# Kernel optimization log

Hardware: AMD Instinct MI355X
Metric: run time of the kernel (lower is better)

## Reference

```python
import jax, jax.numpy as jnp
import numpy as np

DEPTH = 10
LEAF = 2 ** DEPTH          # 1024 leaves
NODE_NUM = 2 * LEAF - 1    # 2047
N = NODE_NUM + 1           # 2048 nodes incl. global node 0
ATTN = 4
D = 128
B = 8
L = 2


def _trace_children(ni):
    terms = []
    s, e = ni << 1, (ni << 1) | 1
    while s <= NODE_NUM and e <= NODE_NUM:
        terms.extend(range(s, e + 1))
        s <<= 1
        e = (e << 1) | 1
    return terms


def _trace_left(si):
    ni, cd, terms, stop = si + LEAF, DEPTH, [], False
    while not stop:
        cs = ni - ATTN + 1 - ((ni - ATTN + 1) & 1)
        stop = cs < 2 ** cd
        cs = max(2 ** cd, cs)
        terms.extend(range(cs, ni + 1))
        ni = (cs - 1) >> 1
        cd -= 1
    return terms


def _trace_right(ei):
    ni, cd, terms, stop = ei + LEAF, DEPTH, [], False
    while not stop:
        ce = ni + ATTN - 1 + ((ni - ATTN) & 1)
        stop = ce >= 2 ** (cd + 1)
        ce = min(2 ** (cd + 1) - 1, ce)
        terms.extend(range(ni, ce + 1))
        ni = (ce + 1) >> 1
        cd -= 1
    return terms


def _build_edges():
    src, dst = [], []
    for ni in range(1, NODE_NUM + 1):
        if ni < LEAF:
            t = _trace_children(ni)
        else:
            t = _trace_left(ni - LEAF) + _trace_right(ni - LEAF)
        src.extend(t)
        dst.extend([ni] * len(t))
    e = np.stack([np.asarray(src, np.int64), np.asarray(dst, np.int64)])  # [2, E]
    off = np.arange(B, dtype=np.int64) * N
    eb = (e[:, None, :] + off[None, :, None]).reshape(2, -1)  # batch-offset like _fetch_edge_data
    return eb.astype(np.int32)


def setup_inputs() -> dict:
    key = jax.random.key(0)
    k0, k1, k2 = jax.random.split(key, 3)
    s = 1.0 / np.sqrt(D)
    return {
        "elements": jax.random.normal(k0, (B, LEAF, D), jnp.float32),
        "ln_gamma": jnp.ones((L, D), jnp.float32),
        "ln_beta": jnp.zeros((L, D), jnp.float32),
        "w_nei": (jax.random.normal(k1, (L, D, D), jnp.float32) * s),
        "b_nei": jnp.zeros((L, D), jnp.float32),
        "w_root": (jax.random.normal(k2, (L, D, D), jnp.float32) * s),
        "edge_index": jnp.asarray(_build_edges()),
    }


def _sinusoid(pos, d):
    # ArbitraryPositionEncoder: sinusoidal encoding over (possibly negative) positions
    half = d // 2
    inv = jnp.exp(-jnp.arange(half, dtype=jnp.float32) * (np.log(10000.0) / half))
    ang = pos[:, None] * inv[None, :]  # [n, half]
    return jnp.stack([jnp.sin(ang), jnp.cos(ang)], -1).reshape(pos.shape[0], d)


def reference(elements, ln_gamma, ln_beta, w_nei, b_nei, w_root, edge_index):
    Bx, leaf, d = elements.shape
    depth = int(np.log2(leaf))
    # bottom-up tree compression (mean of two children)
    cur = elements
    levels = [cur]
    for _ in range(depth):
        cur = 0.5 * (cur[:, 0::2] + cur[:, 1::2])
        levels.append(cur)
    # node ordering: [global node 0 (=-1), root (level 0), ..., leaves (level depth)]
    node_feat = jnp.concatenate(
        [jnp.full((Bx, 1, d), -1.0, elements.dtype)] + levels[::-1], axis=1)  # [B, N, D]
    n = node_feat.shape[1]
    # positional encoding: vertical = floor(log2(idx)), horizontal = idx - 2^vertical
    idx = jnp.arange(n, dtype=jnp.float32)
    vpos = jnp.floor(jnp.log2(jnp.where(idx == 0, 0.5, idx)))
    hpos = idx - jnp.exp2(vpos)
    enc = jnp.concatenate([_sinusoid(hpos, d // 2), _sinusoid(vpos, d // 2)], -1)  # [N, D]
    x = (node_feat + enc[None]).reshape(Bx * n, d)
    src, dst = edge_index[0], edge_index[1]
    nseg = Bx * n
    deg = jnp.maximum(
        jax.ops.segment_sum(jnp.ones(src.shape, jnp.float32), dst, num_segments=nseg), 1.0)
    # DeepGCNLayer res+ blocks with SAGEConv (mean aggr)
    for l in range(ln_gamma.shape[0]):
        mu = jnp.mean(x, -1, keepdims=True)
        var = jnp.mean((x - mu) ** 2, -1, keepdims=True)
        h = (x - mu) * jax.lax.rsqrt(var + 1e-5) * ln_gamma[l] + ln_beta[l]
        h = jax.nn.gelu(h, approximate=False)
        agg = jax.ops.segment_sum(h[src], dst, num_segments=nseg) / deg[:, None]
        h = agg @ w_nei[l] + b_nei[l] + h @ w_root[l]
        x = x + h
    return x.reshape(Bx, n, d)
```

## Files before the change

kernel.cpp:

```cpp
#include <hip/hip_runtime.h>
#include <hip/hip_bf16.h>

#define LEAFN 1024
#define NN    2048
#define BATCH 8
#define DD    128
#define ROWS  (BATCH*NN)
#define AHS   384
#define NB    256
#define NT    1024

#define LOG1E4_OVER_32 0.28782313662425575f

#define SLACK 9
#define CSTRIDE 136
#define AGGL_OFF 54672
#define RED_OFF  63376
#define RED2_OFF 64400

typedef __bf16 bf16x8 __attribute__((ext_vector_type(8)));
typedef float  floatx4 __attribute__((ext_vector_type(4)));
typedef float  floatx2 __attribute__((ext_vector_type(2)));

__device__ __forceinline__ float bf2f(unsigned short u) {
// ... 144 lines not shown
      float4 q0 = *(float4*)rowp;
      float4 q1 = *(float4*)(rowp + 4);
      float4 q2 = *(float4*)(rowp + 8);
      float4 q3 = *(float4*)(rowp + 12);
      float v[16] = {q0.x, q0.y, q0.z, q0.w, q1.x, q1.y, q1.z, q1.w,
                     q2.x, q2.y, q2.z, q2.w, q3.x, q3.y, q3.z, q3.w};
      float s1 = 0.f, s2 = 0.f;
#pragma unroll
      for (int j = 0; j < 16; ++j) { s1 += v[j]; s2 += v[j] * v[j]; }
      s1 += __shfl_xor(s1, 1); s2 += __shfl_xor(s2, 1);
      s1 += __shfl_xor(s1, 2); s2 += __shfl_xor(s2, 2);
      s1 += __shfl_xor(s1, 4); s2 += __shfl_xor(s2, 4);
      float mu = s1 * (1.0f / 128.0f);
      float var = s2 * (1.0f / 128.0f) - mu * mu;
      float rinv = rsqrtf(var + 1e-5f);
      int k = rr + 1, lv = 31 - __clz(k);
      int g = ((16 + s) << lv) | (k - (1 << lv));
      __attribute__((aligned(16))) unsigned short o[16];
      float hv[16];
#pragma unroll
      for (int j = 0; j < 16; ++j) {
        hv[j] = gelu((v[j] - mu) * rinv * gamma[dp + j] + beta[dp + j]);
        o[j] = f2bf(hv[j]);
      }
      *(float4*)rowp        = make_float4(hv[0], hv[1], hv[2], hv[3]);
      *(float4*)(rowp + 4)  = make_float4(hv[4], hv[5], hv[6], hv[7]);
      *(float4*)(rowp + 8)  = make_float4(hv[8], hv[9], hv[10], hv[11]);
      *(float4*)(rowp + 12) = make_float4(hv[12], hv[13], hv[14], hv[15]);
      unsigned short* dst = &ah[(size_t)(b * NN + g) * AHS + 128 + dp];
      *(uint4*)&dst[0] = *(uint4*)&o[0];
      *(uint4*)&dst[8] = *(uint4*)&o[8];
    }
  }
  __syncthreads();
  for (int lv = 5; lv >= 0; --lv) {
    int nk = 1 << lv;
    float inv = 1.0f / (float)((1 << (7 - lv)) - 2);
    for (int idx = tid; idx < nk * 32; idx += NT) {
      int k = nk + (idx >> 5);
      int j = idx & 31;
      floatx4 S = smv[(2 * k - 1) * 32 + j] + smv[(2 * k) * 32 + j];
      if (lv < 5) S = S + smv[(4 * k - 1) * 32 + j] + smv[(4 * k + 1) * 32 + j];
      smv[(2 * k - 1) * 32 + j] = S;
      int g = ((16 + s) << lv) | (k - nk);
      ushort4 o;
      o.x = f2bf(S[0] * inv); o.y = f2bf(S[1] * inv);
      o.z = f2bf(S[2] * inv); o.w = f2bf(S[3] * inv);
      *(ushort4*)&ah[(size_t)(b * NN + g) * AHS + j * 4] = o;
    }
    __syncthreads();
  }
  if (tid < 32)
    ((floatx4*)&sroot[(size_t)(b * 16 + s) * DD])[tid] = smv[32 + tid];
}

__device__ __forceinline__ void ph_top(char* smemc, int b,
                                       const float* __restrict__ lvl4,
                                       unsigned short* __restrict__ ah,
                                       const float* __restrict__ gamma,
                                       const float* __restrict__ beta) {
  float (*xs)[DD] = (float(*)[DD])smemc;
  int tid = threadIdx.x;
  if (tid < 128) {
    int d = tid;
    float v[16];
    for (int j = 0; j < 16; ++j) v[j] = lvl4[(b * 16 + j) * DD + d];
    for (int j = 0; j < 8; ++j) v[j] = 0.5f * (v[2 * j] + v[2 * j + 1]);
    for (int j = 0; j < 8; ++j) xs[8 + j][d] = v[j] + enc_val(8 + j, d);
    for (int j = 0; j < 4; ++j) v[j] = 0.5f * (v[2 * j] + v[2 * j + 1]);
    for (int j = 0; j < 4; ++j) xs[4 + j][d] = v[j] + enc_val(4 + j, d);
    for (int j = 0; j < 2; ++j) v[j] = 0.5f * (v[2 * j] + v[2 * j + 1]);
    for (int j = 0; j < 2; ++j) xs[2 + j][d] = v[j] + enc_val(2 + j, d);
    v[0] = 0.5f * (v[0] + v[1]);
    xs[1][d] = v[0] + enc_val(1, d);
    xs[0][d] = -1.0f + enc_val(0, d);
  }
  __syncthreads();
  if (tid < 128) {
    int rr = tid >> 3, sub = tid & 7, dp = sub * 16;
    float w[16], s1 = 0.f, s2 = 0.f;
#pragma unroll
    for (int j = 0; j < 16; ++j) { w[j] = xs[rr][dp + j]; s1 += w[j]; s2 += w[j] * w[j]; }
    s1 += __shfl_xor(s1, 1); s2 += __shfl_xor(s2, 1);
    s1 += __shfl_xor(s1, 2); s2 += __shfl_xor(s2, 2);
    s1 += __shfl_xor(s1, 4); s2 += __shfl_xor(s2, 4);
    float mu = s1 * (1.0f / 128.0f);
    float var = s2 * (1.0f / 128.0f) - mu * mu;
    float rinv = rsqrtf(var + 1e-5f);
    __attribute__((aligned(16))) unsigned short o[16];
#pragma unroll
    for (int j = 0; j < 16; ++j)
      o[j] = f2bf(gelu((w[j] - mu) * rinv * gamma[dp + j] + beta[dp + j]));
    unsigned short* dst = &ah[(size_t)(b * NN + rr) * AHS + 128 + dp];
    *(uint4*)&dst[0] = *(uint4*)&o[0];
    *(uint4*)&dst[8] = *(uint4*)&o[8];
  }
  __syncthreads();
}

__device__ __forceinline__ void ph_aggsub(char* smemc, int b, int s,
                                          unsigned short* ah,
                                          float* __restrict__ sroot) {
  floatx4 (*S)[32] = (floatx4(*)[32])smemc;
  int tid = threadIdx.x;
  for (int idx = tid; idx < 32 * 32; idx += NT) {
    int k = 32 + (idx >> 5), q = idx & 31;
    int c = (16 + s) * 64 + (2 * k - 64);
    size_t a0 = (size_t)(b * NN + c) * AHS + 256 + q * 4;
    ushort4 u0 = *(const ushort4*)&ah[a0];
    ushort4 u1 = *(const ushort4*)&ah[a0 + AHS];
    floatx4 v;
    v[0] = bf2f(u0.x) + bf2f(u1.x);
    v[1] = bf2f(u0.y) + bf2f(u1.y);
    v[2] = bf2f(u0.z) + bf2f(u1.z);
    v[3] = bf2f(u0.w) + bf2f(u1.w);
    S[k][q] = v;
    int g = (16 + s) * 32 + (k - 32);
    int r = b * NN + g;
    ushort4 o;
    o.x = f2bf(v[0] * 0.5f); o.y = f2bf(v[1] * 0.5f);
    o.z = f2bf(v[2] * 0.5f); o.w = f2bf(v[3] * 0.5f);
    *(ushort4*)&ah[(size_t)r * AHS + q * 4] = o;
  }
  __syncthreads();
  for (int lv = 4; lv >= 0; --lv) {
    int nk = 1 << lv;
    float inv = 1.0f / (float)((1 << (7 - lv)) - 2);
    for (int idx = tid; idx < nk * 32; idx += NT) {
      int k = nk + (idx >> 5), q = idx & 31;
      int c = ((16 + s) << (lv + 1)) | (2 * k - 2 * nk);
      size_t a0 = (size_t)(b * NN + c) * AHS + 256 + q * 4;
      ushort4 u0 = *(const ushort4*)&ah[a0];
      ushort4 u1 = *(const ushort4*)&ah[a0 + AHS];
      floatx4 sc0 = S[2 * k][q], sc1 = S[2 * k + 1][q];
      floatx4 v;
      v[0] = bf2f(u0.x) + bf2f(u1.x) + sc0[0] + sc1[0];
      v[1] = bf2f(u0.y) + bf2f(u1.y) + sc0[1] + sc1[1];
      v[2] = bf2f(u0.z) + bf2f(u1.z) + sc0[2] + sc1[2];
      v[3] = bf2f(u0.w) + bf2f(u1.w) + sc0[3] + sc1[3];
      S[k][q] = v;
      int g = ((16 + s) << lv) | (k - nk);
      int r = b * NN + g;
      ushort4 o;
      o.x = f2bf(v[0] * inv); o.y = f2bf(v[1] * inv);
      o.z = f2bf(v[2] * inv); o.w = f2bf(v[3] * inv);
      *(ushort4*)&ah[(size_t)r * AHS + q * 4] = o;
    }
    __syncthreads();
  }
  for (int q = tid; q < 32; q += NT)
    ((floatx4*)sroot)[(size_t)(b * 16 + s) * 32 + q] = S[1][q];
}

__device__ __forceinline__ void ph_leafagg(char* smemc, int b, int jb,
                                           const int* __restrict__ srcv,
                                           const int* __restrict__ s0a,
                                           const int* __restrict__ s1a,
                                           const unsigned short* __restrict__ eoff,
                                           unsigned short* ah, int hoff) {
  unsigned short* cache = (unsigned short*)smemc;
  int tid = threadIdx.x;
  int lo[11], wd[11], off[11];
  int acc_off = 0;
#pragma unroll
  for (int cd = 10; cd >= 1; --cd) {
    win_cd(jb, cd, lo[cd], wd[cd]);
    off[cd] = acc_off;
    acc_off += wd[cd];
  }
#pragma unroll
  for (int cd = 10; cd >= 1; --cd) {
    int w = wd[cd];
    for (int t = tid; t < w * 16; t += NT) {
      int row = t >> 4, seg = t & 15;
      *(uint4*)&cache[(off[cd] + row) * CSTRIDE + seg * 8] =
          *(const uint4*)&ah[(size_t)(b * NN + lo[cd] + row) * AHS + hoff + seg * 8];
    }
  }
  __syncthreads();

  int leaf = tid >> 5, half = (tid >> 4) & 1, c = tid & 15;
  int r = b * NN + 1024 + jb * 32 + leaf;
  int e0 = s0a[r], e1 = s1a[r];
  int n = e1 - e0;
  int mid = e0 + (n >> 1);
  int ebeg = half ? mid : e0;
  int eend = half ? e1 : mid;
  int cb = c * 16;
  floatx2 a0 = {0.f, 0.f}, a1 = {0.f, 0.f}, a2 = {0.f, 0.f}, a3 = {0.f, 0.f};
  auto one = [&](int ei) {
    unsigned o = eoff[ei];
    uint4 u;
    if (o != 0xFFFFu)
      u = *(const uint4*)(smemc + o + cb);
    else {
      int g = srcv[ei] - b * NN;
      u = *(const uint4*)&ah[(size_t)(b * NN + g) * AHS + hoff + c * 8];
    }
    a0 += bfpair(u.x); a1 += bfpair(u.y); a2 += bfpair(u.z); a3 += bfpair(u.w);
  };
  int e = ebeg;
  for (; e + 4 <= eend; e += 4) {
    unsigned o0 = eoff[e], o1 = eoff[e + 1], o2 = eoff[e + 2], o3 = eoff[e + 3];
    if (!((((o0 + 1) | (o1 + 1) | (o2 + 1) | (o3 + 1)) >> 16))) {
      uint4 u0 = *(const uint4*)(smemc + o0 + cb);
      uint4 u1 = *(const uint4*)(smemc + o1 + cb);
      uint4 u2 = *(const uint4*)(smemc + o2 + cb);
      uint4 u3 = *(const uint4*)(smemc + o3 + cb);
      a0 += bfpair(u0.x); a1 += bfpair(u0.y); a2 += bfpair(u0.z); a3 += bfpair(u0.w);
      a0 += bfpair(u1.x); a1 += bfpair(u1.y); a2 += bfpair(u1.z); a3 += bfpair(u1.w);
      a0 += bfpair(u2.x); a1 += bfpair(u2.y); a2 += bfpair(u2.z); a3 += bfpair(u2.w);
      a0 += bfpair(u3.x); a1 += bfpair(u3.y); a2 += bfpair(u3.z); a3 += bfpair(u3.w);
    } else {
      one(e); one(e + 1); one(e + 2); one(e + 3);
    }
  }
  for (; e < eend; ++e) one(e);
  a0[0] += __shfl_xor(a0[0], 16); a0[1] += __shfl_xor(a0[1], 16);
  a1[0] += __shfl_xor(a1[0], 16); a1[1] += __shfl_xor(a1[1], 16);
  a2[0] += __shfl_xor(a2[0], 16); a2[1] += __shfl_xor(a2[1], 16);
  a3[0] += __shfl_xor(a3[0], 16); a3[1] += __shfl_xor(a3[1], 16);
  if (!half) {
    float inv = 1.0f / (float)max(n, 1);
    unsigned short* aggl = (unsigned short*)(smemc + AGGL_OFF);
    __attribute__((aligned(16))) unsigned short o[8];
    o[0] = f2bf(a0[0] * inv); o[1] = f2bf(a0[1] * inv);
    o[2] = f2bf(a1[0] * inv); o[3] = f2bf(a1[1] * inv);
    o[4] = f2bf(a2[0] * inv); o[5] = f2bf(a2[1] * inv);
    o[6] = f2bf(a3[0] * inv); o[7] = f2bf(a3[1] * inv);
    *(uint4*)&aggl[leaf * CSTRIDE + c * 8] = *(uint4*)&o[0];
  }
}

__device__ __forceinline__ void ph_topfin(int b,
                                          const float* __restrict__ sroot,
                                          unsigned short* ah, int hoff) {
  int d = threadIdx.x;
  float S16[16], h16[16], Sv[16];
#pragma unroll
  for (int j = 0; j < 16; ++j) S16[j] = sroot[(size_t)(b * 16 + j) * DD + d];
#pragma unroll
  for (int j = 0; j < 16; ++j)
    h16[j] = bf2f(ah[(size_t)(b * NN + 16 + j) * AHS + hoff + d]);
#pragma unroll
  for (int k = 8; k < 16; ++k)
    Sv[k] = h16[2 * k - 16] + h16[2 * k - 15] + S16[2 * k - 16] + S16[2 * k - 15];
#pragma unroll
  for (int k = 7; k >= 1; --k)
    Sv[k] = bf2f(ah[(size_t)(b * NN + 2 * k) * AHS + hoff + d]) +
            bf2f(ah[(size_t)(b * NN + 2 * k + 1) * AHS + hoff + d]) +
            Sv[2 * k] + Sv[2 * k + 1];
#pragma unroll
  for (int k = 1; k < 16; ++k) {
    int dv = 31 - __clz(k);
    float inv = 1.0f / (float)((1 << (11 - dv)) - 2);
    ah[(size_t)(b * NN + k) * AHS + d] = f2bf(Sv[k] * inv);
  }
  ah[(size_t)(b * NN) * AHS + d] = f2bf(0.0f);
}

__device__ __forceinline__ void ph_gemm32(char* redc, const unsigned short* aggl,
                                          int rowbase, unsigned short* ah,
                                          const unsigned short* __restrict__ wfl,
                                          const float* __restrict__ bn,
                                          float* __restrict__ x, int hoff_in,
                                          const float* __restrict__ gamma,
                                          const float* __restrict__ beta,
                                          float* xc, int first_layer) {
  int wave = threadIdx.x >> 6, lane = threadIdx.x & 63;
  bool act = wave < 8;
  int wl = wave & 7;
  int mt = wl >> 2, nq = wl & 3;
  int r0 = rowbase + mt * 16;
  int m = lane & 15, q = lane >> 4;
  floatx4 acc[2];
  acc[0] = (floatx4){0.f, 0.f, 0.f, 0.f};
  acc[1] = (floatx4){0.f, 0.f, 0.f, 0.f};
  if (act) {
    const unsigned short* arow = ah + (size_t)(r0 + m) * AHS + q * 8;
    const bf16x8* B = (const bf16x8*)wfl + lane;
#pragma unroll
    for (int kc = 0; kc < 8; ++kc) {
      bf16x8 a0;
      if (kc < 4)
        a0 = *(const bf16x8*)&aggl[(mt * 16 + m) * CSTRIDE + kc * 32 + q * 8];
      else
        a0 = *(const bf16x8*)(arow + hoff_in + (kc - 4) * 32);
#pragma unroll
      for (int ci = 0; ci < 2; ++ci) {
        bf16x8 bb = B[(kc * 8 + nq * 2 + ci) * 64];
        acc[ci] = __builtin_amdgcn_mfma_f32_16x16x32_bf16(a0, bb, acc[ci], 0, 0, 0);
      }
    }
  }
  if (first_layer) {
    float s1[4] = {0.f, 0.f, 0.f, 0.f}, s2[4] = {0.f, 0.f, 0.f, 0.f};
    if (act) {
#pragma unroll
      for (int ci = 0; ci < 2; ++ci) {
        int col = (nq * 2 + ci) * 16 + m;
        float bias = bn[col];
#pragma unroll
        for (int r = 0; r < 4; ++r) {
          int row = r0 + q * 4 + r;
          float v = x[(size_t)row * DD + col] + acc[ci][r] + bias;
          xc[ci * 4 + r] = v;
          s1[r] += v; s2[r] += v * v;
        }
      }
#pragma unroll
      for (int r = 0; r < 4; ++r) {
        s1[r] += __shfl_xor(s1[r], 1); s2[r] += __shfl_xor(s2[r], 1);
        s1[r] += __shfl_xor(s1[r], 2); s2[r] += __shfl_xor(s2[r], 2);
        s1[r] += __shfl_xor(s1[r], 4); s2[r] += __shfl_xor(s2[r], 4);
        s1[r] += __shfl_xor(s1[r], 8); s2[r] += __shfl_xor(s2[r], 8);
      }
    }
    float* red = (float*)redc;
    int rl = mt * 16 + q * 4;
    __syncthreads();
    if (act && m == 0) {
#pragma unroll
      for (int r = 0; r < 4; ++r) {
        red[(rl + r) * 4 + nq] = s1[r];
        red[128 + (rl + r) * 4 + nq] = s2[r];
      }
    }
    __syncthreads();
    if (act) {
      float mu[4], rv[4];
#pragma unroll
      for (int r = 0; r < 4; ++r) {
        float t1 = red[(rl + r) * 4] + red[(rl + r) * 4 + 1] +
                   red[(rl + r) * 4 + 2] + red[(rl + r) * 4 + 3];
        float t2 = red[128 + (rl + r) * 4] + red[128 + (rl + r) * 4 + 1] +
                   red[128 + (rl + r) * 4 + 2] + red[128 + (rl + r) * 4 + 3];
        mu[r] = t1 * (1.0f / 128.0f);
        float var = t2 * (1.0f / 128.0f) - mu[r] * mu[r];
        rv[r] = rsqrtf(var + 1e-5f);
      }
#pragma unroll
      for (int ci = 0; ci < 2; ++ci) {
        int col = (nq * 2 + ci) * 16 + m;
        float gm = gamma[col], bt = beta[col];
#pragma unroll
        for (int r = 0; r < 4; ++r) {
          int row = r0 + q * 4 + r;
          float hh = gelu((xc[ci * 4 + r] - mu[r]) * rv[r] * gm + bt);
          ah[(size_t)row * AHS + 256 + col] = f2bf(hh);
        }
      }
    }
  } else {
    if (act) {
#pragma unroll
      for (int ci = 0; ci < 2; ++ci) {
        int col = (nq * 2 + ci) * 16 + m;
        float bias = bn[col];
#pragma unroll
        for (int r = 0; r < 4; ++r) {
          int row = r0 + q * 4 + r;
          x[(size_t)row * DD + col] = xc[ci * 4 + r] + acc[ci][r] + bias;
        }
      }
    }
  }
}

__device__ __forceinline__ void ph_gemm32s(char* redc, int b, int sb, int tbase,
                                           unsigned short* ah,
                                           const unsigned short* __restrict__ wfl,
                                           const float* __restrict__ bn,
                                           float* __restrict__ x, int hoff_in,
                                           const float* __restrict__ gamma,
                                           const float* __restrict__ beta,
                                           float* xc, int first_layer,
                                           const float* __restrict__ gx) {
  int wave = threadIdx.x >> 6, lane = threadIdx.x & 63;
  bool act = wave >= 8;
  int wl = wave & 7;
  int mt = wl >> 2, nq = wl & 3;
  int m = lane & 15, q = lane >> 4;
  int tA = tbase + mt * 16 + m;
  int kA = (tA == 63) ? 1 : tA + 1;
  int lvA = 31 - __clz(kA);
  int rowA = b * NN + (((16 + sb) << lvA) | (kA - (1 << lvA)));
  int rowO[4];
#pragma unroll
  for (int r = 0; r < 4; ++r) {
    int t = tbase + mt * 16 + q * 4 + r;
    int k = (t == 63) ? 1 : t + 1;
    int lv = 31 - __clz(k);
    rowO[r] = b * NN + (((16 + sb) << lv) | (k - (1 << lv)));
  }
  floatx4 acc[2];
  acc[0] = (floatx4){0.f, 0.f, 0.f, 0.f};
  acc[1] = (floatx4){0.f, 0.f, 0.f, 0.f};
  if (act) {
    const unsigned short* arow = ah + (size_t)rowA * AHS + q * 8;
    const bf16x8* B = (const bf16x8*)wfl + lane;
#pragma unroll
    for (int kc = 0; kc < 8; ++kc) {
      int koff = (kc < 4) ? kc * 32 : hoff_in + (kc - 4) * 32;
      bf16x8 a0 = *(const bf16x8*)(arow + koff);
#pragma unroll
      for (int ci = 0; ci < 2; ++ci) {
        bf16x8 bb = B[(kc * 8 + nq * 2 + ci) * 64];
        acc[ci] = __builtin_amdgcn_mfma_f32_16x16x32_bf16(a0, bb, acc[ci], 0, 0, 0);
      }
    }
  }
  if (first_layer) {
    float s1[4] = {0.f, 0.f, 0.f, 0.f}, s2[4] = {0.f, 0.f, 0.f, 0.f};
    if (act) {
#pragma unroll
      for (int ci = 0; ci < 2; ++ci) {
        int col = (nq * 2 + ci) * 16 + m;
        float bias = bn[col];
#pragma unroll
        for (int r = 0; r < 4; ++r) {
          float x0 = gx ? gx[(size_t)rowO[r] * DD + col] : xc[ci * 4 + r];
          float v = x0 + acc[ci][r] + bias;
          xc[ci * 4 + r] = v;
          s1[r] += v; s2[r] += v * v;
        }
      }
#pragma unroll
      for (int r = 0; r < 4; ++r) {
        s1[r] += __shfl_xor(s1[r], 1); s2[r] += __shfl_xor(s2[r], 1);
        s1[r] += __shfl_xor(s1[r], 2); s2[r] += __shfl_xor(s2[r], 2);
        s1[r] += __shfl_xor(s1[r], 4); s2[r] += __shfl_xor(s2[r], 4);
        s1[r] += __shfl_xor(s1[r], 8); s2[r] += __shfl_xor(s2[r], 8);
      }
    }
    float* red = (float*)redc;
    int rl = mt * 16 + q * 4;
    __syncthreads();
    if (act && m == 0) {
#pragma unroll
      for (int r = 0; r < 4; ++r) {
        red[(rl + r) * 4 + nq] = s1[r];
        red[128 + (rl + r) * 4 + nq] = s2[r];
      }
    }
    __syncthreads();
    if (act) {
      float mu[4], rv[4];
#pragma unroll
      for (int r = 0; r < 4; ++r) {
        float t1 = red[(rl + r) * 4] + red[(rl + r) * 4 + 1] +
                   red[(rl + r) * 4 + 2] + red[(rl + r) * 4 + 3];
        float t2 = red[128 + (rl + r) * 4] + red[128 + (rl + r) * 4 + 1] +
                   red[128 + (rl + r) * 4 + 2] + red[128 + (rl + r) * 4 + 3];
        mu[r] = t1 * (1.0f / 128.0f);
        float var = t2 * (1.0f / 128.0f) - mu[r] * mu[r];
        rv[r] = rsqrtf(var + 1e-5f);
      }
#pragma unroll
      for (int ci = 0; ci < 2; ++ci) {
        int col = (nq * 2 + ci) * 16 + m;
        float gm = gamma[col], bt = beta[col];
#pragma unroll
        for (int r = 0; r < 4; ++r) {
          float hh = gelu((xc[ci * 4 + r] - mu[r]) * rv[r] * gm + bt);
          ah[(size_t)rowO[r] * AHS + 256 + col] = f2bf(hh);
        }
      }
    }
  } else {
    if (act) {
#pragma unroll
      for (int ci = 0; ci < 2; ++ci) {
        int col = (nq * 2 + ci) * 16 + m;
        float bias = bn[col];
#pragma unroll
        for (int r = 0; r < 4; ++r)
          x[(size_t)rowO[r] * DD + col] = xc[ci * 4 + r] + acc[ci][r] + bias;
      }
    }
  }
}

__device__ __forceinline__ void ph_gemm16t(char* redc, int b,
                                           unsigned short* ah,
                                           const unsigned short* __restrict__ wfl,
                                           const float* __restrict__ bn,
                                           float* __restrict__ x, int hoff_in,
                                           const float* __restrict__ gamma,
                                           const float* __restrict__ beta,
                                           float* xc, int first_layer) {
  int ct = threadIdx.x >> 6, lane = threadIdx.x & 63;
  bool act = ct < 8;
  int m = lane & 15, q = lane >> 4;
  floatx4 acc = (floatx4){0.f, 0.f, 0.f, 0.f};
  int col = (ct & 7) * 16 + m;
  if (act) {
    const unsigned short* arow = ah + (size_t)(b * NN + m) * AHS + q * 8;
    const bf16x8* B = (const bf16x8*)wfl + lane;
#pragma unroll
    for (int kc = 0; kc < 8; ++kc) {
      int koff = (kc < 4) ? kc * 32 : hoff_in + (kc - 4) * 32;
      bf16x8 a0 = *(const bf16x8*)(arow + koff);
      bf16x8 bb = B[(kc * 8 + ct) * 64];
      acc = __builtin_amdgcn_mfma_f32_16x16x32_bf16(a0, bb, acc, 0, 0, 0);
    }
  }
  if (first_layer) {
    float s1[4] = {0.f, 0.f, 0.f, 0.f}, s2[4] = {0.f, 0.f, 0.f, 0.f};
    float bias = act ? bn[col] : 0.f;
    if (act) {
#pragma unroll
      for (int r = 0; r < 4; ++r) {
        float v = xc[r] + acc[r] + bias;
        xc[r] = v; s1[r] = v; s2[r] = v * v;
      }
#pragma unroll
      for (int r = 0; r < 4; ++r) {
        s1[r] += __shfl_xor(s1[r], 1); s2[r] += __shfl_xor(s2[r], 1);
        s1[r] += __shfl_xor(s1[r], 2); s2[r] += __shfl_xor(s2[r], 2);
        s1[r] += __shfl_xor(s1[r], 4); s2[r] += __shfl_xor(s2[r], 4);
        s1[r] += __shfl_xor(s1[r], 8); s2[r] += __shfl_xor(s2[r], 8);
      }
    }
    float* red = (float*)redc;
    __syncthreads();
    if (act && m == 0) {
#pragma unroll
      for (int r = 0; r < 4; ++r) {
        red[(q * 4 + r) * 8 + ct] = s1[r];
        red[128 + (q * 4 + r) * 8 + ct] = s2[r];
      }
    }
    __syncthreads();
    if (act) {
#pragma unroll
      for (int r = 0; r < 4; ++r) {
        float t1 = 0.f, t2 = 0.f;
#pragma unroll
        for (int j = 0; j < 8; ++j) {
          t1 += red[(q * 4 + r) * 8 + j];
          t2 += red[128 + (q * 4 + r) * 8 + j];
        }
        float mu = t1 * (1.0f / 128.0f);
        float var = t2 * (1.0f / 128.0f) - mu * mu;
        float rv = rsqrtf(var + 1e-5f);
        float hh = gelu((xc[r] - mu) * rv * gamma[col] + beta[col]);
        ah[(size_t)(b * NN + q * 4 + r) * AHS + 256 + col] = f2bf(hh);
      }
    }
  } else {
    if (act) {
      float bias = bn[col];
#pragma unroll
      for (int r = 0; r < 4; ++r)
        x[(size_t)(b * NN + q * 4 + r) * DD + col] = xc[r] + acc[r] + bias;
    }
  }
}

__global__ __launch_bounds__(NT, 1) void k_mega(
    const float* __restrict__ elements, const float* __restrict__ ln_gamma,
    const float* __restrict__ ln_beta, const float* __restrict__ w_nei,
    const float* __restrict__ b_nei, const float* __restrict__ w_root,
    const int* __restrict__ srcv, const int* __restrict__ dstv, int E,
    float* __restrict__ x, int* s0a, int* s1a, float* lvl4, float* sroot,
    unsigned short* wf, unsigned short* ah, unsigned short* eoff, int* bar) {
  __shared__ __align__(16) char smem[65536];
  int bid = blockIdx.x, tid = threadIdx.x;
  int b = bid & 7, gb = bid >> 3;
  int Eb = E >> 3;
  unsigned short* wfg = wf + (size_t)b * 65536;
  float xcl[8], xci[8], xct[4];
  int wv = tid >> 6;

  if (gb < 16) {
    ph_tree(smem, b, gb, elements, x, lvl4, ah, ln_gamma, ln_beta, sroot, xci, bar);
  } else if (gb < 24) {
    int base = b * Eb;
    for (int i = base + (gb - 16) * NT + tid; i < base + Eb; i += 8 * NT) {
      int dv = dstv[i];
      if (i == 0 || dstv[i - 1] != dv) s0a[dv] = i;
      if (i == base + Eb - 1 || dstv[i + 1] != dv) s1a[dv] = i + 1;
    }
    for (int i = base + (gb - 16) * NT + tid; i < base + Eb; i += 8 * NT) {
      int dl = dstv[i] - b * NN - 1024;
      unsigned short ov = 0xFFFFu;
      if (dl >= 0) {
        int jb2 = dl >> 5;
        int g = srcv[i] - b * NN;
        int lv = 31 - __clz(g);
        int acc2 = 0;
#pragma unroll
        for (int cd = 10; cd >= 1; --cd) {
          int lo_, wd_;
          win_cd(jb2, cd, lo_, wd_);
          if (cd == lv) {
            int idx = g - lo_;
            if ((unsigned)idx < (unsigned)wd_)
              ov = (unsigned short)((acc2 + idx) * (2 * CSTRIDE));
          }
          acc2 += wd_;
        }
      }
      eoff[i] = ov;
    }
  } else if (gb < 28) {
    int gi = (gb - 24) * NT + tid;
    int lane = gi & 63, ct = (gi >> 6) & 7, kc = gi >> 9;
    int n = ct * 16 + (lane & 15);
    int k = kc * 32 + (lane >> 4) * 8;
    int kk = k & 127;
#pragma unroll
    for (int l = 0; l < 2; ++l) {
      const float* w = (k < 128) ? (w_nei + (size_t)l * DD * DD)
                                 : (w_root + (size_t)l * DD * DD);
      unsigned short* o = wfg + (size_t)l * 32768 + (size_t)gi * 8;
#pragma unroll
      for (int j = 0; j < 8; ++j) o[j] = f2bf(w[(size_t)(kk + j) * DD + n]);
    }
  } else if (gb == 28) {
    if (tid < 16) {
      while (!__hip_atomic_load(bar + 1536 + b * 64 + tid * 4, __ATOMIC_RELAXED,
                                __HIP_MEMORY_SCOPE_AGENT))
        __builtin_amdgcn_s_sleep(1);
      __threadfence();
    }
    __syncthreads();
    ph_top(smem, b, lvl4, ah, ln_gamma, ln_beta);
    {
      int ln = tid & 63, m_ = ln & 15, q_ = ln >> 4;
      if (wv < 8) {
        float (*xs)[DD] = (float(*)[DD])smem;
#pragma unroll
        for (int r = 0; r < 4; ++r) xct[r] = xs[q_ * 4 + r][wv * 16 + m_];
      }
    }
  }
  gbarN(bar, 0);

  if (gb == 28) {
    if (tid < 128) ph_topfin(b, sroot, ah, 128);
    __syncthreads();
    ph_gemm16t(smem + RED_OFF, b, ah, wfg, b_nei, x, 128,
               ln_gamma + DD, ln_beta + DD, xct, 1);
    __syncthreads();
  }
  ph_leafagg(smem, b, gb, srcv, s0a, s1a, eoff, ah, 128);
  __syncthreads();
  if (wv < 8) {
    ph_gemm32(smem + RED_OFF, (const unsigned short*)(smem + AGGL_OFF),
              b * NN + 1024 + gb * 32, ah, wfg, b_nei, x, 128,
              ln_gamma + DD, ln_beta + DD, xcl, 1);
  } else if (gb < 16) {
    ph_gemm32s(smem + RED2_OFF, b, gb, 32, ah, wfg, b_nei, x, 128,
               ln_gamma + DD, ln_beta + DD, xci, 1, nullptr);
  } else {
    ph_gemm32s(smem + RED2_OFF, b, gb - 16, 0, ah, wfg, b_nei, x, 128,
               ln_gamma + DD, ln_beta + DD, xci, 1, x);
  }
  gbarN(bar, 1);

  if (gb < 16) {
    ph_aggsub(smem, b, gb, ah, sroot);
    __syncthreads();
    if (tid == 0) {
      __threadfence();
      __hip_atomic_store(bar + 1024 + b * 64 + gb * 4, 1, __ATOMIC_RELAXED,
                         __HIP_MEMORY_SCOPE_AGENT);
    }
  }
  ph_leafagg(smem, b, gb, srcv, s0a, s1a, eoff, ah, 256);
  if (gb >= 16 && tid == 0) {
    while (!__hip_atomic_load(bar + 1024 + b * 64 + (gb - 16) * 4, __ATOMIC_RELAXED,
                              __HIP_MEMORY_SCOPE_AGENT))
      __builtin_amdgcn_s_sleep(1);
    __threadfence();
  }
  __syncthreads();
  if (wv < 8) {
    ph_gemm32(smem + RED_OFF, (const unsigned short*)(smem + AGGL_OFF),
              b * NN + 1024 + gb * 32, ah, wfg + 32768, b_nei + DD,
              x, 256, ln_gamma, ln_beta, xcl, 0);
  } else if (gb < 16) {
    ph_gemm32s(smem + RED2_OFF, b, gb, 32, ah, wfg + 32768, b_nei + DD, x, 256,
               ln_gamma, ln_beta, xci, 0, nullptr);
  } else {
    ph_gemm32s(smem + RED2_OFF, b, gb - 16, 0, ah, wfg + 32768, b_nei + DD, x, 256,
               ln_gamma, ln_beta, xci, 0, nullptr);
  }
  if (gb == 28) {
    if (tid < 16) {
      while (!__hip_atomic_load(bar + 1024 + b * 64 + tid * 4, __ATOMIC_RELAXED,
                                __HIP_MEMORY_SCOPE_AGENT))
        __builtin_amdgcn_s_sleep(1);
      __threadfence();
    }
    __syncthreads();
    if (tid < 128) ph_topfin(b, sroot, ah, 256);
    __syncthreads();
    ph_gemm16t(smem + RED_OFF, b, ah, wfg + 32768, b_nei + DD, x, 256,
               ln_gamma, ln_beta, xct, 0);
  }
}

extern "C" void kernel_launch(void* const* d_in, const int* in_sizes, int n_in,
                              void* d_out, int out_size, void* d_ws, size_t ws_size,
                              hipStream_t stream) {
  const float* elements = (const float*)d_in[0];
  const float* ln_gamma = (const float*)d_in[1];
  const float* ln_beta  = (const float*)d_in[2];
  const float* w_nei    = (const float*)d_in[3];
  const float* b_nei    = (const float*)d_in[4];
  const float* w_root   = (const float*)d_in[5];
  const int*   edge     = (const int*)d_in[6];
  int E = in_sizes[6] / 2;
  const int* srcv = edge;
  const int* dstv = edge + E;
  float* x = (float*)d_out;

  char* ws = (char*)d_ws;
  int*            bar   = (int*)ws;
  int*            s0    = (int*)(ws + 65536);
  int*            s1    = (int*)(ws + 131072);
  float*          lvl4  = (float*)(ws + 196608);
  float*          sroot = (float*)(ws + 262144);
  unsigned short* wf    = (unsigned short*)(ws + 327680);
  unsigned short* ah    = (unsigned short*)(ws + 327680 + 1048576);
  unsigned short* eoff  = (unsigned short*)(ws + 327680 + 1048576 + 12582912);

  hipMemsetAsync(bar, 0, 8192, stream);
  k_mega<<<dim3(NB), dim3(NT), 0, stream>>>(
      elements, ln_gamma, ln_beta, w_nei, b_nei, w_root,
      srcv, dstv, E, x, s0, s1, lvl4, sroot, wf, ah, eoff, bar);
}
```

Measured before the change: 163.4 us.

## Split block into leaf-aggregation and internal-GEMM wave groups running concurrently

The 1024-thread block is divided so waves 0-7 stage the window, gather the leaf neighbours (one thread per 8-column slice per leaf, no half-split shuffle) and run the leaf GEMM. Waves 8-15 concurrently run the internal-node GEMM and layernorm, split into part1/part2 functions. Previously all 16 waves did the leaf aggregation first and only then split for the GEMMs. The x residual loads are also hoisted ahead of the MFMA loops. In exchange the gather now runs on half the threads, and the __syncthreads calls in the two branches must pair up in matching counts to stay correct.

```diff
diff --git a/kernel.cpp b/kernel.cpp
--- a/kernel.cpp
+++ b/kernel.cpp
@@ -320,12 +320,9 @@
     ((floatx4*)sroot)[(size_t)(b * 16 + s) * 32 + q] = S[1][q];
 }
 
-__device__ __forceinline__ void ph_leafagg(char* smemc, int b, int jb,
-                                           const int* __restrict__ srcv,
-                                           const int* __restrict__ s0a,
-                                           const int* __restrict__ s1a,
-                                           const unsigned short* __restrict__ eoff,
-                                           unsigned short* ah, int hoff) {
+__device__ __forceinline__ void ph_stage(char* smemc, int b, int jb,
+                                         const unsigned short* __restrict__ ah,
+                                         int hoff) {
   unsigned short* cache = (unsigned short*)smemc;
   int tid = threadIdx.x;
   int lo[11], wd[11], off[11];
@@ -339,21 +336,25 @@
 #pragma unroll
   for (int cd = 10; cd >= 1; --cd) {
     int w = wd[cd];
-    for (int t = tid; t < w * 16; t += NT) {
+    for (int t = tid; t < w * 16; t += 512) {
       int row = t >> 4, seg = t & 15;
       *(uint4*)&cache[(off[cd] + row) * CSTRIDE + seg * 8] =
           *(const uint4*)&ah[(size_t)(b * NN + lo[cd] + row) * AHS + hoff + seg * 8];
     }
   }
-  __syncthreads();
-
-  int leaf = tid >> 5, half = (tid >> 4) & 1, c = tid & 15;
+}
+
+__device__ __forceinline__ void ph_gather(char* smemc, int b, int jb,
+                                          const int* __restrict__ srcv,
+                                          const int* __restrict__ s0a,
+                                          const int* __restrict__ s1a,
+                                          const unsigned short* __restrict__ eoff,
+                                          const unsigned short* __restrict__ ah,
+                                          int hoff) {
+  int tid = threadIdx.x;
+  int leaf = tid >> 4, c = tid & 15;
   int r = b * NN + 1024 + jb * 32 + leaf;
   int e0 = s0a[r], e1 = s1a[r];
-  int n = e1 - e0;
-  int mid = e0 + (n >> 1);
-  int ebeg = half ? mid : e0;
-  int eend = half ? e1 : mid;
   int cb = c * 16;
   floatx2 a0 = {0.f, 0.f}, a1 = {0.f, 0.f}, a2 = {0.f, 0.f}, a3 = {0.f, 0.f};
   auto one = [&](int ei) {
@@ -367,8 +368,8 @@
     }
     a0 += bfpair(u.x); a1 += bfpair(u.y); a2 += bfpair(u.z); a3 += bfpair(u.w);
   };
-  int e = ebeg;
-  for (; e + 4 <= eend; e += 4) {
+  int e = e0;
+  for (; e + 4 <= e1; e += 4) {
     unsigned o0 = eoff[e], o1 = eoff[e + 1], o2 = eoff[e + 2], o3 = eoff[e + 3];
     if (!((((o0 + 1) | (o1 + 1) | (o2 + 1) | (o3 + 1)) >> 16))) {
       uint4 u0 = *(const uint4*)(smemc + o0 + cb);
@@ -383,21 +384,15 @@
       one(e); one(e + 1); one(e + 2); one(e + 3);
     }
   }
-  for (; e < eend; ++e) one(e);
-  a0[0] += __shfl_xor(a0[0], 16); a0[1] += __shfl_xor(a0[1], 16);
-  a1[0] += __shfl_xor(a1[0], 16); a1[1] += __shfl_xor(a1[1], 16);
-  a2[0] += __shfl_xor(a2[0], 16); a2[1] += __shfl_xor(a2[1], 16);
-  a3[0] += __shfl_xor(a3[0], 16); a3[1] += __shfl_xor(a3[1], 16);
-  if (!half) {
-    float inv = 1.0f / (float)max(n, 1);
-    unsigned short* aggl = (unsigned short*)(smemc + AGGL_OFF);
-    __attribute__((aligned(16))) unsigned short o[8];
-    o[0] = f2bf(a0[0] * inv); o[1] = f2bf(a0[1] * inv);
-    o[2] = f2bf(a1[0] * inv); o[3] = f2bf(a1[1] * inv);
-    o[4] = f2bf(a2[0] * inv); o[5] = f2bf(a2[1] * inv);
-    o[6] = f2bf(a3[0] * inv); o[7] = f2bf(a3[1] * inv);
-    *(uint4*)&aggl[leaf * CSTRIDE + c * 8] = *(uint4*)&o[0];
-  }
+  for (; e < e1; ++e) one(e);
+  float inv = 1.0f / (float)max(e1 - e0, 1);
+  unsigned short* aggl = (unsigned short*)(smemc + AGGL_OFF);
+  __attribute__((aligned(16))) unsigned short o[8];
+  o[0] = f2bf(a0[0] * inv); o[1] = f2bf(a0[1] * inv);
+  o[2] = f2bf(a1[0] * inv); o[3] = f2bf(a1[1] * inv);
+  o[4] = f2bf(a2[0] * inv); o[5] = f2bf(a2[1] * inv);
+  o[6] = f2bf(a3[0] * inv); o[7] = f2bf(a3[1] * inv);
+  *(uint4*)&aggl[leaf * CSTRIDE + c * 8] = *(uint4*)&o[0];
 }
 
 __device__ __forceinline__ void ph_topfin(int b,
@@ -427,133 +422,116 @@
   ah[(size_t)(b * NN) * AHS + d] = f2bf(0.0f);
 }
 
-__device__ __forceinline__ void ph_gemm32(char* redc, const unsigned short* aggl,
-                                          int rowbase, unsigned short* ah,
-                                          const unsigned short* __restrict__ wfl,
-                                          const float* __restrict__ bn,
-                                          float* __restrict__ x, int hoff_in,
-                                          const float* __restrict__ gamma,
-                                          const float* __restrict__ beta,
-                                          float* xc, int first_layer) {
-  int wave = threadIdx.x >> 6, lane = threadIdx.x & 63;
-  bool act = wave < 8;
-  int wl = wave & 7;
-  int mt = wl >> 2, nq = wl & 3;
-  int r0 = rowbase + mt * 16;
-  int m = lane & 15, q = lane >> 4;
-  floatx4 acc[2];
-  acc[0] = (floatx4){0.f, 0.f, 0.f, 0.f};
-  acc[1] = (floatx4){0.f, 0.f, 0.f, 0.f};
-  if (act) {
-    const unsigned short* arow = ah + (size_t)(r0 + m) * AHS + q * 8;
-    const bf16x8* B = (const bf16x8*)wfl + lane;
-#pragma unroll
-    for (int kc = 0; kc < 8; ++kc) {
-      bf16x8 a0;
-      if (kc < 4)
-        a0 = *(const bf16x8*)&aggl[(mt * 16 + m) * CSTRIDE + kc * 32 + q * 8];
-      else
-        a0 = *(const bf16x8*)(arow + hoff_in + (kc - 4) * 32);
-#pragma unroll
-      for (int ci = 0; ci < 2; ++ci) {
-        bf16x8 bb = B[(kc * 8 + nq * 2 + ci) * 64];
-        acc[ci] = __builtin_amdgcn_mfma_f32_16x16x32_bf16(a0, bb, acc[ci], 0, 0, 0);
-      }
-    }
-  }
-  if (first_layer) {
-    float s1[4] = {0.f, 0.f, 0.f, 0.f}, s2[4] = {0.f, 0.f, 0.f, 0.f};
-    if (act) {
-#pragma unroll
-      for (int ci = 0; ci < 2; ++ci) {
-        int col = (nq * 2 + ci) * 16 + m;
-        float bias = bn[col];
-#pragma unroll
-        for (int r = 0; r < 4; ++r) {
-          int row = r0 + q * 4 + r;
-          float v = x[(size_t)row * DD + col] + acc[ci][r] + bias;
-          xc[ci * 4 + r] = v;
-          s1[r] += v; s2[r] += v * v;
-        }
-      }
-#pragma unroll
-      for (int r = 0; r < 4; ++r) {
-        s1[r] += __shfl_xor(s1[r], 1); s2[r] += __shfl_xor(s2[r], 1);
-        s1[r] += __shfl_xor(s1[r], 2); s2[r] += __shfl_xor(s2[r], 2);
-        s1[r] += __shfl_xor(s1[r], 4); s2[r] += __shfl_xor(s2[r], 4);
-        s1[r] += __shfl_xor(s1[r], 8); s2[r] += __shfl_xor(s2[r], 8);
-      }
-    }
-    float* red = (float*)redc;
-    int rl = mt * 16 + q * 4;
-    __syncthreads();
-    if (act && m == 0) {
-#pragma unroll
-      for (int r = 0; r < 4; ++r) {
-        red[(rl + r) * 4 + nq] = s1[r];
-        red[128 + (rl + r) * 4 + nq] = s2[r];
-      }
-    }
-    __syncthreads();
-    if (act) {
-      float mu[4], rv[4];
-#pragma unroll
-      for (int r = 0; r < 4; ++r) {
-        float t1 = red[(rl + r) * 4] + red[(rl + r) * 4 + 1] +
-                   red[(rl + r) * 4 + 2] + red[(rl + r) * 4 + 3];
-        float t2 = red[128 + (rl + r) * 4] + red[128 + (rl + r) * 4 + 1] +
-                   red[128 + (rl + r) * 4 + 2] + red[128 + (rl + r) * 4 + 3];
-        mu[r] = t1 * (1.0f / 128.0f);
-        float var = t2 * (1.0f / 128.0f) - mu[r] * mu[r];
-        rv[r] = rsqrtf(var + 1e-5f);
-      }
-#pragma unroll
-      for (int ci = 0; ci < 2; ++ci) {
-        int col = (nq * 2 + ci) * 16 + m;
-        float gm = gamma[col], bt = beta[col];
-#pragma unroll
-        for (int r = 0; r < 4; ++r) {
-          int row = r0 + q * 4 + r;
-          float hh = gelu((xc[ci * 4 + r] - mu[r]) * rv[r] * gm + bt);
-          ah[(size_t)row * AHS + 256 + col] = f2bf(hh);
-        }
-      }
-    }
-  } else {
-    if (act) {
-#pragma unroll
-      for (int ci = 0; ci < 2; ++ci) {
-        int col = (nq * 2 + ci) * 16 + m;
-        float bias = bn[col];
-#pragma unroll
-        for (int r = 0; r < 4; ++r) {
-          int row = r0 + q * 4 + r;
-          x[(size_t)row * DD + col] = xc[ci * 4 + r] + acc[ci][r] + bias;
-        }
-      }
-    }
-  }
-}
-
-__device__ __forceinline__ void ph_gemm32s(char* redc, int b, int sb, int tbase,
-                                           unsigned short* ah,
+__device__ __forceinline__ void ph_gemm32L(char* redc, const unsigned short* aggl,
+                                           int rowbase, unsigned short* ah,
                                            const unsigned short* __restrict__ wfl,
                                            const float* __restrict__ bn,
                                            float* __restrict__ x, int hoff_in,
                                            const float* __restrict__ gamma,
                                            const float* __restrict__ beta,
-                                           float* xc, int first_layer,
-                                           const float* __restrict__ gx) {
+                                           float* xc, int first_layer) {
   int wave = threadIdx.x >> 6, lane = threadIdx.x & 63;
-  bool act = wave >= 8;
-  int wl = wave & 7;
-  int mt = wl >> 2, nq = wl & 3;
+  int mt = wave >> 2, nq = wave & 3;
+  int r0 = rowbase + mt * 16;
   int m = lane & 15, q = lane >> 4;
+  float xpre[8];
+  if (first_layer) {
+#pragma unroll
+    for (int ci = 0; ci < 2; ++ci)
+#pragma unroll
+      for (int r = 0; r < 4; ++r)
+        xpre[ci * 4 + r] = x[(size_t)(r0 + q * 4 + r) * DD + (nq * 2 + ci) * 16 + m];
+  }
+  const unsigned short* arow = ah + (size_t)(r0 + m) * AHS + q * 8;
+  const bf16x8* B = (const bf16x8*)wfl + lane;
+  floatx4 acc[2];
+  acc[0] = (floatx4){0.f, 0.f, 0.f, 0.f};
+  acc[1] = (floatx4){0.f, 0.f, 0.f, 0.f};
+#pragma unroll
+  for (int kc = 0; kc < 8; ++kc) {
+    bf16x8 a0;
+    if (kc < 4)
+      a0 = *(const bf16x8*)&aggl[(mt * 16 + m) * CSTRIDE + kc * 32 + q * 8];
+    else
+      a0 = *(const bf16x8*)(arow + hoff_in + (kc - 4) * 32);
+#pragma unroll
+    for (int ci = 0; ci < 2; ++ci) {
+      bf16x8 bb = B[(kc * 8 + nq * 2 + ci) * 64];
+      acc[ci] = __builtin_amdgcn_mfma_f32_16x16x32_bf16(a0, bb, acc[ci], 0, 0, 0);
+    }
+  }
+  if (first_layer) {
+    float s1[4] = {0.f, 0.f, 0.f, 0.f}, s2[4] = {0.f, 0.f, 0.f, 0.f};
+#pragma unroll
+    for (int ci = 0; ci < 2; ++ci) {
+      int col = (nq * 2 + ci) * 16 + m;
+      float bias = bn[col];
+#pragma unroll
+      for (int r = 0; r < 4; ++r) {
+        float v = xpre[ci * 4 + r] + acc[ci][r] + bias;
+        xc[ci * 4 + r] = v;
+        s1[r] += v; s2[r] += v * v;
+      }
+    }
+#pragma unroll
+    for (int r = 0; r < 4; ++r) {
+      s1[r] += __shfl_xor(s1[r], 1); s2[r] += __shfl_xor(s2[r], 1);
+      s1[r] += __shfl_xor(s1[r], 2); s2[r] += __shfl_xor(s2[r], 2);
+      s1[r] += __shfl_xor(s1[r], 4); s2[r] += __shfl_xor(s2[r], 4);
+      s1[r] += __shfl_xor(s1[r], 8); s2[r] += __shfl_xor(s2[r], 8);
+    }
+    float* red = (float*)redc;
+    int rl = mt * 16 + q * 4;
+    if (m == 0) {
+#pragma unroll
+      for (int r = 0; r < 4; ++r) {
+        red[(rl + r) * 4 + nq] = s1[r];
+        red[128 + (rl + r) * 4 + nq] = s2[r];
+      }
+    }
+    __syncthreads();
+    float mu[4], rv[4];
+#pragma unroll
+    for (int r = 0; r < 4; ++r) {
+      float t1 = red[(rl + r) * 4] + red[(rl + r) * 4 + 1] +
+                 red[(rl + r) * 4 + 2] + red[(rl + r) * 4 + 3];
+      float t2 = red[128 + (rl + r) * 4] + red[128 + (rl + r) * 4 + 1] +
+                 red[128 + (rl + r) * 4 + 2] + red[128 + (rl + r) * 4 + 3];
+      mu[r] = t1 * (1.0f / 128.0f);
+      float var = t2 * (1.0f / 128.0f) - mu[r] * mu[r];
+      rv[r] = rsqrtf(var + 1e-5f);
+    }
+#pragma unroll
+    for (int ci = 0; ci < 2; ++ci) {
+      int col = (nq * 2 + ci) * 16 + m;
+      float gm = gamma[col], bt = beta[col];
+#pragma unroll
+      for (int r = 0; r < 4; ++r) {
+        int row = r0 + q * 4 + r;
+        float hh = gelu((xc[ci * 4 + r] - mu[r]) * rv[r] * gm + bt);
+        ah[(size_t)row * AHS + 256 + col] = f2bf(hh);
+      }
+    }
+  } else {
+#pragma unroll
+    for (int ci = 0; ci < 2; ++ci) {
+      int col = (nq * 2 + ci) * 16 + m;
+      float bias = bn[col];
+#pragma unroll
+      for (int r = 0; r < 4; ++r) {
+        int row = r0 + q * 4 + r;
+        x[(size_t)row * DD + col] = xc[ci * 4 + r] + acc[ci][r] + bias;
+      }
+    }
+  }
+}
+
+__device__ __forceinline__ void g32s_rows(int b, int sb, int tbase, int mt,
+                                          int m, int q, int& rowA, int* rowO) {
   int tA = tbase + mt * 16 + m;
   int kA = (tA == 63) ? 1 : tA + 1;
   int lvA = 31 - __clz(kA);
-  int rowA = b * NN + (((16 + sb) << lvA) | (kA - (1 << lvA)));
-  int rowO[4];
+  rowA = b * NN + (((16 + sb) << lvA) | (kA - (1 << lvA)));
 #pragma unroll
   for (int r = 0; r < 4; ++r) {
     int t = tbase + mt * 16 + q * 4 + r;
@@ -561,91 +539,137 @@
     int lv = 31 - __clz(k);
     rowO[r] = b * NN + (((16 + sb) << lv) | (k - (1 << lv)));
   }
-  floatx4 acc[2];
+}
+
+__device__ __forceinline__ void g32s_mfma(int rowA, unsigned short* ah,
+                                          const unsigned short* __restrict__ wfl,
+                                          int hoff_in, int nq, int q, int lane,
+                                          floatx4* acc) {
+  const unsigned short* arow = ah + (size_t)rowA * AHS + q * 8;
+  const bf16x8* B = (const bf16x8*)wfl + lane;
   acc[0] = (floatx4){0.f, 0.f, 0.f, 0.f};
   acc[1] = (floatx4){0.f, 0.f, 0.f, 0.f};
-  if (act) {
-    const unsigned short* arow = ah + (size_t)rowA * AHS + q * 8;
-    const bf16x8* B = (const bf16x8*)wfl + lane;
-#pragma unroll
-    for (int kc = 0; kc < 8; ++kc) {
-      int koff = (kc < 4) ? kc * 32 : hoff_in + (kc - 4) * 32;
-      bf16x8 a0 = *(const bf16x8*)(arow + koff);
-#pragma unroll
-      for (int ci = 0; ci < 2; ++ci) {
-        bf16x8 bb = B[(kc * 8 + nq * 2 + ci) * 64];
-        acc[ci] = __builtin_amdgcn_mfma_f32_16x16x32_bf16(a0, bb, acc[ci], 0, 0, 0);
-      }
-    }
-  }
-  if (first_layer) {
-    float s1[4] = {0.f, 0.f, 0.f, 0.f}, s2[4] = {0.f, 0.f, 0.f, 0.f};
-    if (act) {
-#pragma unroll
-      for (int ci = 0; ci < 2; ++ci) {
-        int col = (nq * 2 + ci) * 16 + m;
-        float bias = bn[col];
-#pragma unroll
-        for (int r = 0; r < 4; ++r) {
-          float x0 = gx ? gx[(size_t)rowO[r] * DD + col] : xc[ci * 4 + r];
-          float v = x0 + acc[ci][r] + bias;
-          xc[ci * 4 + r] = v;
-          s1[r] += v; s2[r] += v * v;
-        }
-      }
-#pragma unroll
-      for (int r = 0; r < 4; ++r) {
-        s1[r] += __shfl_xor(s1[r], 1); s2[r] += __shfl_xor(s2[r], 1);
-        s1[r] += __shfl_xor(s1[r], 2); s2[r] += __shfl_xor(s2[r], 2);
-        s1[r] += __shfl_xor(s1[r], 4); s2[r] += __shfl_xor(s2[r], 4);
-        s1[r] += __shfl_xor(s1[r], 8); s2[r] += __shfl_xor(s2[r], 8);
-      }
-    }
-    float* red = (float*)redc;
-    int rl = mt * 16 + q * 4;
-    __syncthreads();
-    if (act && m == 0) {
-#pragma unroll
-      for (int r = 0; r < 4; ++r) {
-        red[(rl + r) * 4 + nq] = s1[r];
-        red[128 + (rl + r) * 4 + nq] = s2[r];
-      }
-    }
-    __syncthreads();
-    if (act) {
-      float mu[4], rv[4];
-#pragma unroll
-      for (int r = 0; r < 4; ++r) {
-        float t1 = red[(rl + r) * 4] + red[(rl + r) * 4 + 1] +
-                   red[(rl + r) * 4 + 2] + red[(rl + r) * 4 + 3];
-        float t2 = red[128 + (rl + r) * 4] + red[128 + (rl + r) * 4 + 1] +
-                   red[128 + (rl + r) * 4 + 2] + red[128 + (rl + r) * 4 + 3];
-        mu[r] = t1 * (1.0f / 128.0f);
-        float var = t2 * (1.0f / 128.0f) - mu[r] * mu[r];
-        rv[r] = rsqrtf(var + 1e-5f);
-      }
-#pragma unroll
-      for (int ci = 0; ci < 2; ++ci) {
-        int col = (nq * 2 + ci) * 16 + m;
-        float gm = gamma[col], bt = beta[col];
-#pragma unroll
-        for (int r = 0; r < 4; ++r) {
-          float hh = gelu((xc[ci * 4 + r] - mu[r]) * rv[r] * gm + bt);
-          ah[(size_t)rowO[r] * AHS + 256 + col] = f2bf(hh);
-        }
-      }
-    }
+#pragma unroll
+  for (int kc = 0; kc < 8; ++kc) {
+    int koff = (kc < 4) ? kc * 32 : hoff_in + (kc - 4) * 32;
+    bf16x8 a0 = *(const bf16x8*)(arow + koff);
+#pragma unroll
+    for (int ci = 0; ci < 2; ++ci) {
+      bf16x8 bb = B[(kc * 8 + nq * 2 + ci) * 64];
+      acc[ci] = __builtin_amdgcn_mfma_f32_16x16x32_bf16(a0, bb, acc[ci], 0, 0, 0);
+    }
+  }
+}
+
+__device__ __forceinline__ void ph_g32s_part1(char* redc, int b, int sb, int tbase,
+                                              unsigned short* ah,
+                                              const unsigned short* __restrict__ wfl,
+                                              const float* __restrict__ bn,
+                                              int hoff_in, float* xc,
+                                              const float* __restrict__ gx) {
+  int wave = threadIdx.x >> 6, lane = threadIdx.x & 63;
+  int wl = wave & 7, mt = wl >> 2, nq = wl & 3;
+  int m = lane & 15, q = lane >> 4;
+  int rowA, rowO[4];
+  g32s_rows(b, sb, tbase, mt, m, q, rowA, rowO);
+  float xpre[8];
+  if (gx) {
+#pragma unroll
+    for (int ci = 0; ci < 2; ++ci)
+#pragma unroll
+      for (int r = 0; r < 4; ++r)
+        xpre[ci * 4 + r] = gx[(size_t)rowO[r] * DD + (nq * 2 + ci) * 16 + m];
   } else {
-    if (act) {
-#pragma unroll
-      for (int ci = 0; ci < 2; ++ci) {
-        int col = (nq * 2 + ci) * 16 + m;
-        float bias = bn[col];
-#pragma unroll
-        for (int r = 0; r < 4; ++r)
-          x[(size_t)rowO[r] * DD + col] = xc[ci * 4 + r] + acc[ci][r] + bias;
-      }
-    }
+#pragma unroll
+    for (int j = 0; j < 8; ++j) xpre[j] = xc[j];
+  }
+  floatx4 acc[2];
+  g32s_mfma(rowA, ah, wfl, hoff_in, nq, q, lane, acc);
+  float s1[4] = {0.f, 0.f, 0.f, 0.f}, s2[4] = {0.f, 0.f, 0.f, 0.f};
+#pragma unroll
+  for (int ci = 0; ci < 2; ++ci) {
+    int col = (nq * 2 + ci) * 16 + m;
+    float bias = bn[col];
+#pragma unroll
+    for (int r = 0; r < 4; ++r) {
+      float v = xpre[ci * 4 + r] + acc[ci][r] + bias;
+      xc[ci * 4 + r] = v;
+      s1[r] += v; s2[r] += v * v;
+    }
+  }
+#pragma unroll
+  for (int r = 0; r < 4; ++r) {
+    s1[r] += __shfl_xor(s1[r], 1); s2[r] += __shfl_xor(s2[r], 1);
+    s1[r] += __shfl_xor(s1[r], 2); s2[r] += __shfl_xor(s2[r], 2);
+    s1[r] += __shfl_xor(s1[r], 4); s2[r] += __shfl_xor(s2[r], 4);
+    s1[r] += __shfl_xor(s1[r], 8); s2[r] += __shfl_xor(s2[r], 8);
+  }
+  float* red = (float*)redc;
+  int rl = mt * 16 + q * 4;
+  if (m == 0) {
+#pragma unroll
+    for (int r = 0; r < 4; ++r) {
+      red[(rl + r) * 4 + nq] = s1[r];
+      red[128 + (rl + r) * 4 + nq] = s2[r];
+    }
+  }
+}
+
+__device__ __forceinline__ void ph_g32s_part2(char* redc, int b, int sb, int tbase,
+                                              unsigned short* ah,
+                                              const float* __restrict__ gamma,
+                                              const float* __restrict__ beta,
+                                              const float* xc) {
+  int wave = threadIdx.x >> 6, lane = threadIdx.x & 63;
+  int wl = wave & 7, mt = wl >> 2, nq = wl & 3;
+  int m = lane & 15, q = lane >> 4;
+  int rowA, rowO[4];
+  g32s_rows(b, sb, tbase, mt, m, q, rowA, rowO);
+  float* red = (float*)redc;
+  int rl = mt * 16 + q * 4;
+  float mu[4], rv[4];
+#pragma unroll
+  for (int r = 0; r < 4; ++r) {
+    float t1 = red[(rl + r) * 4] + red[(rl + r) * 4 + 1] +
+               red[(rl + r) * 4 + 2] + red[(rl + r) * 4 + 3];
+    float t2 = red[128 + (rl + r) * 4] + red[128 + (rl + r) * 4 + 1] +
+               red[128 + (rl + r) * 4 + 2] + red[128 + (rl + r) * 4 + 3];
+    mu[r] = t1 * (1.0f / 128.0f);
+    float var = t2 * (1.0f / 128.0f) - mu[r] * mu[r];
+    rv[r] = rsqrtf(var + 1e-5f);
+  }
+#pragma unroll
+  for (int ci = 0; ci < 2; ++ci) {
+    int col = (nq * 2 + ci) * 16 + m;
+    float gm = gamma[col], bt = beta[col];
+#pragma unroll
+    for (int r = 0; r < 4; ++r) {
+      float hh = gelu((xc[ci * 4 + r] - mu[r]) * rv[r] * gm + bt);
+      ah[(size_t)rowO[r] * AHS + 256 + col] = f2bf(hh);
+    }
+  }
+}
+
+__device__ __forceinline__ void ph_g32s_store(int b, int sb, int tbase,
+                                              unsigned short* ah,
+                                              const unsigned short* __restrict__ wfl,
+                                              const float* __restrict__ bn,
+                                              float* __restrict__ x, int hoff_in,
+                                              const float* xc) {
+  int wave = threadIdx.x >> 6, lane = threadIdx.x & 63;
+  int wl = wave & 7, mt = wl >> 2, nq = wl & 3;
+  int m = lane & 15, q = lane >> 4;
+  int rowA, rowO[4];
+  g32s_rows(b, sb, tbase, mt, m, q, rowA, rowO);
+  floatx4 acc[2];
+  g32s_mfma(rowA, ah, wfl, hoff_in, nq, q, lane, acc);
+#pragma unroll
+  for (int ci = 0; ci < 2; ++ci) {
+    int col = (nq * 2 + ci) * 16 + m;
+    float bias = bn[col];
+#pragma unroll
+    for (int r = 0; r < 4; ++r)
+      x[(size_t)rowO[r] * DD + col] = xc[ci * 4 + r] + acc[ci][r] + bias;
   }
 }
 
@@ -813,18 +837,26 @@
                ln_gamma + DD, ln_beta + DD, xct, 1);
     __syncthreads();
   }
-  ph_leafagg(smem, b, gb, srcv, s0a, s1a, eoff, ah, 128);
-  __syncthreads();
   if (wv < 8) {
-    ph_gemm32(smem + RED_OFF, (const unsigned short*)(smem + AGGL_OFF),
-              b * NN + 1024 + gb * 32, ah, wfg, b_nei, x, 128,
-              ln_gamma + DD, ln_beta + DD, xcl, 1);
-  } else if (gb < 16) {
-    ph_gemm32s(smem + RED2_OFF, b, gb, 32, ah, wfg, b_nei, x, 128,
-               ln_gamma + DD, ln_beta + DD, xci, 1, nullptr);
+    ph_stage(smem, b, gb, ah, 128);
+    __syncthreads();
+    ph_gather(smem, b, gb, srcv, s0a, s1a, eoff, ah, 128);
+    __syncthreads();
+    ph_gemm32L(smem + RED_OFF, (const unsigned short*)(smem + AGGL_OFF),
+               b * NN + 1024 + gb * 32, ah, wfg, b_nei, x, 128,
+               ln_gamma + DD, ln_beta + DD, xcl, 1);
   } else {
-    ph_gemm32s(smem + RED2_OFF, b, gb - 16, 0, ah, wfg, b_nei, x, 128,
-               ln_gamma + DD, ln_beta + DD, xci, 1, x);
+    __syncthreads();
+    if (gb < 16)
+      ph_g32s_part1(smem + RED2_OFF, b, gb, 32, ah, wfg, b_nei, 128, xci, nullptr);
+    else
+      ph_g32s_part1(smem + RED2_OFF, b, gb - 16, 0, ah, wfg, b_nei, 128, xci, x);
+    __syncthreads();
+    if (gb < 16)
+      ph_g32s_part2(smem + RED2_OFF, b, gb, 32, ah, ln_gamma + DD, ln_beta + DD, xci);
+    else
+      ph_g32s_part2(smem + RED2_OFF, b, gb - 16, 0, ah, ln_gamma + DD, ln_beta + DD, xci);
+    __syncthreads();
   }
   gbarN(bar, 1);
 
@@ -837,24 +869,26 @@
                          __HIP_MEMORY_SCOPE_AGENT);
     }
   }
-  ph_leafagg(smem, b, gb, srcv, s0a, s1a, eoff, ah, 256);
-  if (gb >= 16 && tid == 0) {
-    while (!__hip_atomic_load(bar + 1024 + b * 64 + (gb - 16) * 4, __ATOMIC_RELAXED,
-                              __HIP_MEMORY_SCOPE_AGENT))
-      __builtin_amdgcn_s_sleep(1);
-    __threadfence();
-  }
-  __syncthreads();
   if (wv < 8) {
-    ph_gemm32(smem + RED_OFF, (const unsigned short*)(smem + AGGL_OFF),
-              b * NN + 1024 + gb * 32, ah, wfg + 32768, b_nei + DD,
-              x, 256, ln_gamma, ln_beta, xcl, 0);
-  } else if (gb < 16) {
-    ph_gemm32s(smem + RED2_OFF, b, gb, 32, ah, wfg + 32768, b_nei + DD, x, 256,
-               ln_gamma, ln_beta, xci, 0, nullptr);
+    ph_stage(smem, b, gb, ah, 256);
+    __syncthreads();
+    ph_gather(smem, b, gb, srcv, s0a, s1a, eoff, ah, 256);
+    __syncthreads();
+    ph_gemm32L(smem + RED_OFF, (const unsigned short*)(smem + AGGL_OFF),
+               b * NN + 1024 + gb * 32, ah, wfg + 32768, b_nei + DD,
+               x, 256, ln_gamma, ln_beta, xcl, 0);
   } else {
-    ph_gemm32s(smem + RED2_OFF, b, gb - 16, 0, ah, wfg + 32768, b_nei + DD, x, 256,
-               ln_gamma, ln_beta, xci, 0, nullptr);
+    __syncthreads();
+    if (gb >= 16) {
+      while (!__hip_atomic_load(bar + 1024 + b * 64 + (gb - 16) * 4,
+                                __ATOMIC_RELAXED, __HIP_MEMORY_SCOPE_AGENT))
+        __builtin_amdgcn_s_sleep(1);
+      __threadfence();
+      ph_g32s_store(b, gb - 16, 0, ah, wfg + 32768, b_nei + DD, x, 256, xci);
+    } else {
+      ph_g32s_store(b, gb, 32, ah, wfg + 32768, b_nei + DD, x, 256, xci);
+    }
+    __syncthreads();
   }
   if (gb == 28) {
     if (tid < 16) {
```

New measurement: 180.3 us. +10.3%, slower.
